# Performance work log

Hardware: AMD Instinct MI355X
Metric: run time of the kernel (lower is better)

Reference implementation:

```python
import jax, jax.numpy as jnp
import numpy as np

B, L, D_MODEL, D_FF, N_EXPERTS, TOP_K = 32, 256, 512, 2048, 8, 2
EPS = 1e-9


def setup_inputs() -> dict:
    key = jax.random.key(0)
    ks = jax.random.split(key, 7)
    scale1 = 1.0 / np.sqrt(D_MODEL)
    scale2 = 1.0 / np.sqrt(D_FF)
    return {
        "cycle_curve_data": jax.random.normal(ks[0], (B, L, D_MODEL), jnp.float32),
        "logits": jax.random.normal(ks[1], (B, N_EXPERTS), jnp.float32),
        "moe_masks": jax.random.randint(ks[2], (B, N_EXPERTS), 0, 2, jnp.int32),
        "W1": jax.random.normal(ks[3], (N_EXPERTS, D_MODEL, D_FF), jnp.float32) * scale1,
        "b1": jax.random.normal(ks[4], (N_EXPERTS, D_FF), jnp.float32) * scale1,
        "W2": jax.random.normal(ks[5], (N_EXPERTS, D_FF, D_MODEL), jnp.float32) * scale2,
        "b2": jax.random.normal(ks[6], (N_EXPERTS, D_MODEL), jnp.float32) * scale2,
    }


def _gates(logits, moe_masks):
    # softmax over experts, zero out unavailable experts, keep top-k, renormalize
    mask = (moe_masks == 1).astype(logits.dtype)               # [B, E]
    p = jax.nn.softmax(logits, axis=1) * mask                  # [B, E]
    _, idx = jax.lax.top_k(p, TOP_K)                           # [B, K]
    topk_mask = jnp.zeros_like(p).at[jnp.arange(p.shape[0])[:, None], idx].set(1.0)
    p = p * topk_mask
    return p / (jnp.sum(p, axis=1, keepdims=True) + EPS)       # [B, E]


def reference(cycle_curve_data, logits, moe_masks, W1, b1, W2, b2):
    gates = _gates(logits, moe_masks)                          # [B, E]
    x = cycle_curve_data                                       # [B, L, D]
    # dense equivalent of per-expert gather -> MLP -> gate-weighted scatter-combine
    h = jnp.einsum("bld,edf->eblf", x, W1) + b1[:, None, None, :]   # [E,B,L,F]
    h = jax.nn.gelu(h, approximate=False)
    out = jnp.einsum("be,eblf,efd->bld", gates, h, W2)
    out = out + jnp.einsum("be,ed->bd", gates, b2)[:, None, :]      # [B,L,D]
    return out
```

## Files before the change

### kernel.cpp

```cpp
#include <hip/hip_runtime.h>

#define B_SZ 32
#define L_SZ 256
#define D_SZ 512
#define F_SZ 2048
#define E_SZ 8
#define P_SZ 64
#define BK2  32

typedef __attribute__((ext_vector_type(8)))  short bf16x8;
typedef __attribute__((ext_vector_type(16))) float f32x16;

__device__ __forceinline__ unsigned short f2bf(float f) {
  unsigned int u = __builtin_bit_cast(unsigned int, f);
  u += 0x7fffu + ((u >> 16) & 1u);
  return (unsigned short)(u >> 16);
}

__device__ __forceinline__ void async16(const void* g, void* l) {
  __builtin_amdgcn_global_load_lds(
      (const __attribute__((address_space(1))) unsigned int*)g,
      (__attribute__((address_space(3))) unsigned int*)l, 16, 0, 0);
}

__device__ __forceinline__ float gelu_f(float x) {
  float a = fabsf(x) * 0.70710678118654752f;
  float t = __builtin_amdgcn_rcpf(1.0f + 0.3275911f * a);
  float y = t * (0.254829592f +
            t * (-0.284496736f +
            t * (1.421413741f +
            t * (-1.453152027f +
            t * 1.061405429f))));
  float e = __expf(-a * a);
  float erf_abs = 1.0f - y * e;
  float erf_v = (x < 0.f) ? -erf_abs : erf_abs;
  return 0.5f * x * (1.0f + erf_v);
}

#define PREP_CONV_BLKS 4096
#define PREP_TR_BLKS   2048
#define PREP_TOTAL     (1 + PREP_CONV_BLKS + 2 * PREP_TR_BLKS)

__global__ __launch_bounds__(256) void prep_kernel(
    const float* __restrict__ logits, const int* __restrict__ masks,
    const float* __restrict__ x,
    const float* __restrict__ W1, const float* __restrict__ W2,
    int* __restrict__ sel_e, float* __restrict__ sel_g,
    unsigned short* __restrict__ xb,
    unsigned short* __restrict__ w1t, unsigned short* __restrict__ w2t) {
  __shared__ float tile[64][65];
  int blk = blockIdx.x;
  int tid = threadIdx.x;

  if (blk == 0) {
    int b = tid;
    if (b >= B_SZ) return;
    float lg[E_SZ], p[E_SZ];
    float mx = -1e30f;
    for (int e = 0; e < E_SZ; ++e) { lg[e] = logits[b * E_SZ + e]; mx = fmaxf(mx, lg[e]); }
    float s = 0.f;
    for (int e = 0; e < E_SZ; ++e) { p[e] = expf(lg[e] - mx); s += p[e]; }
    for (int e = 0; e < E_SZ; ++e) p[e] = (masks[b * E_SZ + e] == 1) ? (p[e] / s) : 0.f;
    int i0 = 0, i1 = 1; float v0 = -1.f, v1 = -1.f;
    for (int e = 0; e < E_SZ; ++e) {
      float v = p[e];
      if (v > v0)      { v1 = v0; i1 = i0; v0 = v; i0 = e; }
      else if (v > v1) { v1 = v;  i1 = e; }
    }
    float den = v0 + v1 + 1e-9f;
    sel_e[2 * b] = i0;  sel_e[2 * b + 1] = i1;
    sel_g[2 * b] = v0 / den;
    sel_g[2 * b + 1] = v1 / den;
    return;
  }
  blk -= 1;

  if (blk < PREP_CONV_BLKS) {
    int i = blk * 256 + tid;
    float4 v = ((const float4*)x)[i];
    ushort4 o;
    o.x = f2bf(v.x); o.y = f2bf(v.y); o.z = f2bf(v.z); o.w = f2bf(v.w);
    ((ushort4*)xb)[i] = o;
    return;
  }
  blk -= PREP_CONV_BLKS;

  const float* in; unsigned short* out; int R, C, ls;
  if (blk < PREP_TR_BLKS) { in = W1; out = w1t; R = D_SZ; C = F_SZ; ls = 5; }
  else { blk -= PREP_TR_BLKS; in = W2; out = w2t; R = F_SZ; C = D_SZ; ls = 3; }
  int z = blk >> 8;
  int rem = blk & 255;
  int tr = rem >> ls, tc = rem & ((1 << ls) - 1);
  int r0 = tr * 64, c0 = tc * 64;
  const float* ip = in + (size_t)z * R * C;
  unsigned short* op = out + (size_t)z * C * R;
  int tx = tid & 63, ty = tid >> 6;
#pragma unroll
  for (int i = 0; i < 16; ++i) {
    int r = i * 4 + ty;
    tile[r][tx] = ip[(size_t)(r0 + r) * C + c0 + tx];
  }
  __syncthreads();
#pragma unroll
  for (int uu = 0; uu < 4; ++uu) {
    int u = uu * 256 + tid;
    int cc = u >> 4, q = u & 15;
    ushort4 o;
    o.x = f2bf(tile[q * 4 + 0][cc]);
    o.y = f2bf(tile[q * 4 + 1][cc]);
    o.z = f2bf(tile[q * 4 + 2][cc]);
    o.w = f2bf(tile[q * 4 + 3][cc]);
    *(ushort4*)(op + (size_t)(c0 + cc) * R + r0 + q * 4) = o;
  }
}

__global__ __launch_bounds__(256, 4) void moe_gemm1(
    const unsigned short* __restrict__ Xb,
    const unsigned short* __restrict__ W1t,
    const float* __restrict__ b1,
    const int* __restrict__ sel_e,
    unsigned short* __restrict__ H) {
  __shared__ __align__(16) unsigned short As[2][128 * BK2];
  __shared__ __align__(16) unsigned short Bs[2][128 * BK2];

  int lin = blockIdx.x;
  int xcd = lin & 7;
  int f   = (lin >> 3) & 15;
  int grp = lin >> 7;
  int pl  = grp * 8 + xcd;
  int p   = pl >> 1;
  int l0  = (pl & 1) * 128;
  int f0  = f * 128;
  int b   = p >> 1;
  int e   = sel_e[p];

  int tid = threadIdx.x;
  int lane = tid & 63;
  int w = tid >> 6, wm = w & 1, wn = w >> 1;
  int m32 = lane & 31, kh = lane >> 5;

  const unsigned short* Abase = Xb  + ((size_t)b * L_SZ + l0) * D_SZ;
  const unsigned short* Bbase = W1t + ((size_t)e * F_SZ + f0) * D_SZ;

  int seg0 = w * 128 + lane;
  int row0 = seg0 >> 2, ks0 = (seg0 & 3) * 8;
  int seg1 = seg0 + 64;
  int row1 = seg1 >> 2, ks1 = (seg1 & 3) * 8;

  f32x16 acc[2][2] = {};

  for (int k0 = 0; k0 < D_SZ; k0 += 2 * BK2) {
#pragma unroll
    for (int h = 0; h < 2; ++h) {
      int kk = k0 + h * BK2;
      async16(Abase + (size_t)row0 * D_SZ + kk + ks0, &As[h][seg0 * 8]);
      async16(Abase + (size_t)row1 * D_SZ + kk + ks1, &As[h][seg1 * 8]);
      async16(Bbase + (size_t)row0 * D_SZ + kk + ks0, &Bs[h][seg0 * 8]);
      async16(Bbase + (size_t)row1 * D_SZ + kk + ks1, &Bs[h][seg1 * 8]);
    }
    __syncthreads();
#pragma unroll
    for (int h = 0; h < 2; ++h)
#pragma unroll
      for (int s = 0; s < 2; ++s) {
        int ko = s * 16 + kh * 8;
        bf16x8 a0 = *(const bf16x8*)&As[h][(wm * 64 +      m32) * BK2 + ko];
        bf16x8 a1 = *(const bf16x8*)&As[h][(wm * 64 + 32 + m32) * BK2 + ko];
        bf16x8 b0 = *(const bf16x8*)&Bs[h][(wn * 64 +      m32) * BK2 + ko];
        bf16x8 b1f = *(const bf16x8*)&Bs[h][(wn * 64 + 32 + m32) * BK2 + ko];
        acc[0][0] = __builtin_amdgcn_mfma_f32_32x32x16_bf16(a0, b0,  acc[0][0], 0, 0, 0);
        acc[0][1] = __builtin_amdgcn_mfma_f32_32x32x16_bf16(a0, b1f, acc[0][1], 0, 0, 0);
        acc[1][0] = __builtin_amdgcn_mfma_f32_32x32x16_bf16(a1, b0,  acc[1][0], 0, 0, 0);
        acc[1][1] = __builtin_amdgcn_mfma_f32_32x32x16_bf16(a1, b1f, acc[1][1], 0, 0, 0);
      }
    __syncthreads();
  }

  float b1v[2];
#pragma unroll
  for (int tj = 0; tj < 2; ++tj)
    b1v[tj] = b1[e * F_SZ + f0 + wn * 64 + tj * 32 + m32];

  unsigned short* Hp = H + ((size_t)p * L_SZ + l0) * F_SZ + f0;
#pragma unroll
  for (int ti = 0; ti < 2; ++ti)
#pragma unroll
    for (int tj = 0; tj < 2; ++tj) {
      int col = wn * 64 + tj * 32 + m32;
#pragma unroll
      for (int r = 0; r < 16; ++r) {
        int row = wm * 64 + ti * 32 + (r & 3) + 8 * (r >> 2) + 4 * kh;
        Hp[(size_t)row * F_SZ + col] = f2bf(gelu_f(acc[ti][tj][r] + b1v[tj]));
      }
    }
}

__global__ __launch_bounds__(256, 4) void moe_gemm2(
    const unsigned short* __restrict__ H,
    const unsigned short* __restrict__ W2t,
    const float* __restrict__ b2,
    const int* __restrict__ sel_e,
    const float* __restrict__ sel_g,
    float* __restrict__ part,
    float* __restrict__ Out) {
  __shared__ __align__(16) unsigned short As[2][128 * BK2];
  __shared__ __align__(16) unsigned short Bs[2][128 * BK2];

  int lin = blockIdx.x;
  int q   = lin & 7;
  int d   = (lin >> 3) & 3;
  int g8  = lin >> 5;
  int gg  = g8 * 8 + q;
  int p   = gg >> 1;
  int l0  = (gg & 1) * 128;
  int d0  = d * 128;
  int b   = p >> 1;
  int e   = sel_e[p];
  float g = sel_g[p];

  int tid = threadIdx.x;
  int lane = tid & 63;
  int w = tid >> 6, wm = w & 1, wn = w >> 1;
  int m32 = lane & 31, kh = lane >> 5;

  const unsigned short* Abase = H   + ((size_t)p * L_SZ + l0) * F_SZ;
  const unsigned short* Bbase = W2t + ((size_t)e * D_SZ + d0) * F_SZ;

  int seg0 = w * 128 + lane;
  int row0 = seg0 >> 2, ks0 = (seg0 & 3) * 8;
  int seg1 = seg0 + 64;
  int row1 = seg1 >> 2, ks1 = (seg1 & 3) * 8;

  f32x16 acc[2][2] = {};

  for (int k0 = 0; k0 < F_SZ; k0 += 2 * BK2) {
#pragma unroll
    for (int h = 0; h < 2; ++h) {
      int kk = k0 + h * BK2;
      async16(Abase + (size_t)row0 * F_SZ + kk + ks0, &As[h][seg0 * 8]);
      async16(Abase + (size_t)row1 * F_SZ + kk + ks1, &As[h][seg1 * 8]);
      async16(Bbase + (size_t)row0 * F_SZ + kk + ks0, &Bs[h][seg0 * 8]);
      async16(Bbase + (size_t)row1 * F_SZ + kk + ks1, &Bs[h][seg1 * 8]);
    }
    __syncthreads();
#pragma unroll
    for (int h = 0; h < 2; ++h)
#pragma unroll
      for (int s = 0; s < 2; ++s) {
        int ko = s * 16 + kh * 8;
        bf16x8 a0 = *(const bf16x8*)&As[h][(wm * 64 +      m32) * BK2 + ko];
        bf16x8 a1 = *(const bf16x8*)&As[h][(wm * 64 + 32 + m32) * BK2 + ko];
        bf16x8 b0 = *(const bf16x8*)&Bs[h][(wn * 64 +      m32) * BK2 + ko];
        bf16x8 b1f = *(const bf16x8*)&Bs[h][(wn * 64 + 32 + m32) * BK2 + ko];
        acc[0][0] = __builtin_amdgcn_mfma_f32_32x32x16_bf16(a0, b0,  acc[0][0], 0, 0, 0);
        acc[0][1] = __builtin_amdgcn_mfma_f32_32x32x16_bf16(a0, b1f, acc[0][1], 0, 0, 0);
        acc[1][0] = __builtin_amdgcn_mfma_f32_32x32x16_bf16(a1, b0,  acc[1][0], 0, 0, 0);
        acc[1][1] = __builtin_amdgcn_mfma_f32_32x32x16_bf16(a1, b1f, acc[1][1], 0, 0, 0);
      }
    __syncthreads();
  }

  float bias[2] = {0.f, 0.f};
  if (p & 1) {
    int e0 = sel_e[2 * b], e1 = sel_e[2 * b + 1];
    float g0 = sel_g[2 * b], g1 = sel_g[2 * b + 1];
#pragma unroll
    for (int tj = 0; tj < 2; ++tj) {
      int dd = d0 + wn * 64 + tj * 32 + m32;
      bias[tj] = g0 * b2[e0 * D_SZ + dd] + g1 * b2[e1 * D_SZ + dd];
    }
  }
  float* dst = (p & 1) ? Out : part;
  float* Op = dst + ((size_t)b * L_SZ + l0) * D_SZ + d0;
#pragma unroll
  for (int ti = 0; ti < 2; ++ti)
#pragma unroll
    for (int tj = 0; tj < 2; ++tj) {
      int col = wn * 64 + tj * 32 + m32;
#pragma unroll
      for (int r = 0; r < 16; ++r) {
        int row = wm * 64 + ti * 32 + (r & 3) + 8 * (r >> 2) + 4 * kh;
        Op[(size_t)row * D_SZ + col] = g * acc[ti][tj][r] + bias[tj];
      }
    }
}

__global__ __launch_bounds__(256) void combine_kernel(
    const float* __restrict__ part, float* __restrict__ Out) {
  int i = blockIdx.x * 256 + threadIdx.x;
  float4 pv = ((const float4*)part)[i];
  float4 o  = ((float4*)Out)[i];
  o.x += pv.x; o.y += pv.y; o.z += pv.z; o.w += pv.w;
  ((float4*)Out)[i] = o;
}

extern "C" void kernel_launch(void* const* d_in, const int* in_sizes, int n_in,
                              void* d_out, int out_size, void* d_ws, size_t ws_size,
                              hipStream_t stream) {
  const float* x      = (const float*)d_in[0];
  const float* logits = (const float*)d_in[1];
  const int*   masks  = (const int*)d_in[2];
  const float* W1     = (const float*)d_in[3];
  const float* b1     = (const float*)d_in[4];
  const float* W2     = (const float*)d_in[5];
  const float* b2     = (const float*)d_in[6];
  float* out = (float*)d_out;

  char* ws = (char*)d_ws;
  int*   sel_e = (int*)ws;
  float* sel_g = (float*)(ws + 256);
  unsigned short* xb  = (unsigned short*)(ws + 1024);
  unsigned short* w1t = xb  + (size_t)B_SZ * L_SZ * D_SZ;
  unsigned short* w2t = w1t + (size_t)E_SZ * F_SZ * D_SZ;
  unsigned short* Hbuf = w2t + (size_t)E_SZ * D_SZ * F_SZ;
  float* part = (float*)(ws + 1024);

  prep_kernel<<<PREP_TOTAL, 256, 0, stream>>>(logits, masks, x, W1, W2,
                                              sel_e, sel_g, xb, w1t, w2t);
  moe_gemm1<<<2048, 256, 0, stream>>>(xb, w1t, b1, sel_e, Hbuf);
  moe_gemm2<<<512, 256, 0, stream>>>(Hbuf, w2t, b2, sel_e, sel_g, part, out);
  combine_kernel<<<(B_SZ * L_SZ * D_SZ / 4) / 256, 256, 0, stream>>>(part, out);
}
```

Baseline: 245.5 us.

## Overlap W2 transpose with GEMM1 and swizzle LDS tiles to avoid bank conflicts

Moves the W2 fp32-to-bf16 transpose out of the prep kernel and into extra blocks appended to the GEMM1 launch, so that work runs alongside GEMM1 instead of serially before it. Adds an XOR swizzle on the LDS k-chunk layout in both GEMMs to cut bank conflicts on the bf16x8 fragment reads. Also simplifies the GEMM1 block-to-tile mapping by dropping the XCD-aware remap. The tail transpose blocks use GEMM1's 32KB shared buffer and may compete with GEMM blocks for occupancy, and losing the XCD mapping may hurt L2 locality.

After: 226.1 us. 1.09x faster.

```diff
diff --git a/kernel.cpp b/kernel.cpp
--- a/kernel.cpp
+++ b/kernel.cpp
@@ -37,18 +37,41 @@
   return 0.5f * x * (1.0f + erf_v);
 }
 
+__device__ __forceinline__ void transpose_tile(
+    const float* __restrict__ ip, unsigned short* __restrict__ op,
+    int R, int C, int r0, int c0, float* tile, int tid) {
+  int tx = tid & 63, ty = tid >> 6;
+#pragma unroll
+  for (int i = 0; i < 16; ++i) {
+    int r = i * 4 + ty;
+    tile[r * 65 + tx] = ip[(size_t)(r0 + r) * C + c0 + tx];
+  }
+  __syncthreads();
+#pragma unroll
+  for (int uu = 0; uu < 4; ++uu) {
+    int u = uu * 256 + tid;
+    int cc = u >> 4, q = u & 15;
+    ushort4 o;
+    o.x = f2bf(tile[(q * 4 + 0) * 65 + cc]);
+    o.y = f2bf(tile[(q * 4 + 1) * 65 + cc]);
+    o.z = f2bf(tile[(q * 4 + 2) * 65 + cc]);
+    o.w = f2bf(tile[(q * 4 + 3) * 65 + cc]);
+    *(ushort4*)(op + (size_t)(c0 + cc) * R + r0 + q * 4) = o;
+  }
+}
+
 #define PREP_CONV_BLKS 4096
 #define PREP_TR_BLKS   2048
-#define PREP_TOTAL     (1 + PREP_CONV_BLKS + 2 * PREP_TR_BLKS)
+#define PREP_TOTAL     (1 + PREP_CONV_BLKS + PREP_TR_BLKS)
 
 __global__ __launch_bounds__(256) void prep_kernel(
     const float* __restrict__ logits, const int* __restrict__ masks,
     const float* __restrict__ x,
-    const float* __restrict__ W1, const float* __restrict__ W2,
+    const float* __restrict__ W1,
     int* __restrict__ sel_e, float* __restrict__ sel_g,
     unsigned short* __restrict__ xb,
-    unsigned short* __restrict__ w1t, unsigned short* __restrict__ w2t) {
-  __shared__ float tile[64][65];
+    unsigned short* __restrict__ w1t) {
+  __shared__ float tile[64 * 65];
   int blk = blockIdx.x;
   int tid = threadIdx.x;
 
@@ -85,33 +108,11 @@
   }
   blk -= PREP_CONV_BLKS;
 
-  const float* in; unsigned short* out; int R, C, ls;
-  if (blk < PREP_TR_BLKS) { in = W1; out = w1t; R = D_SZ; C = F_SZ; ls = 5; }
-  else { blk -= PREP_TR_BLKS; in = W2; out = w2t; R = F_SZ; C = D_SZ; ls = 3; }
   int z = blk >> 8;
   int rem = blk & 255;
-  int tr = rem >> ls, tc = rem & ((1 << ls) - 1);
-  int r0 = tr * 64, c0 = tc * 64;
-  const float* ip = in + (size_t)z * R * C;
-  unsigned short* op = out + (size_t)z * C * R;
-  int tx = tid & 63, ty = tid >> 6;
-#pragma unroll
-  for (int i = 0; i < 16; ++i) {
-    int r = i * 4 + ty;
-    tile[r][tx] = ip[(size_t)(r0 + r) * C + c0 + tx];
-  }
-  __syncthreads();
-#pragma unroll
-  for (int uu = 0; uu < 4; ++uu) {
-    int u = uu * 256 + tid;
-    int cc = u >> 4, q = u & 15;
-    ushort4 o;
-    o.x = f2bf(tile[q * 4 + 0][cc]);
-    o.y = f2bf(tile[q * 4 + 1][cc]);
-    o.z = f2bf(tile[q * 4 + 2][cc]);
-    o.w = f2bf(tile[q * 4 + 3][cc]);
-    *(ushort4*)(op + (size_t)(c0 + cc) * R + r0 + q * 4) = o;
-  }
+  int tr = rem >> 5, tc = rem & 31;
+  transpose_tile(W1 + (size_t)z * D_SZ * F_SZ, w1t + (size_t)z * D_SZ * F_SZ,
+                 D_SZ, F_SZ, tr * 64, tc * 64, tile, tid);
 }
 
 __global__ __launch_bounds__(256, 4) void moe_gemm1(
@@ -119,33 +120,45 @@
     const unsigned short* __restrict__ W1t,
     const float* __restrict__ b1,
     const int* __restrict__ sel_e,
-    unsigned short* __restrict__ H) {
-  __shared__ __align__(16) unsigned short As[2][128 * BK2];
-  __shared__ __align__(16) unsigned short Bs[2][128 * BK2];
-
+    unsigned short* __restrict__ H,
+    const float* __restrict__ W2,
+    unsigned short* __restrict__ w2t) {
+  __shared__ __align__(16) char smem[32768];
+  int tid = threadIdx.x;
   int lin = blockIdx.x;
-  int xcd = lin & 7;
-  int f   = (lin >> 3) & 15;
-  int grp = lin >> 7;
-  int pl  = grp * 8 + xcd;
-  int p   = pl >> 1;
-  int l0  = (pl & 1) * 128;
-  int f0  = f * 128;
-  int b   = p >> 1;
-  int e   = sel_e[p];
-
-  int tid = threadIdx.x;
+
+  if (lin >= 2048) {
+    int blk = lin - 2048;
+    int z = blk >> 8;
+    int rem = blk & 255;
+    int tr = rem >> 3, tc = rem & 7;
+    transpose_tile(W2 + (size_t)z * F_SZ * D_SZ, w2t + (size_t)z * F_SZ * D_SZ,
+                   F_SZ, D_SZ, tr * 64, tc * 64, (float*)smem, tid);
+    return;
+  }
+
+  unsigned short* As = (unsigned short*)smem;
+  unsigned short* Bs = (unsigned short*)(smem + 16384);
+
+  int f  = lin & 15;
+  int l0 = ((lin >> 4) & 1) * 128;
+  int p  = lin >> 5;
+  int f0 = f * 128;
+  int b  = p >> 1;
+  int e  = sel_e[p];
+
   int lane = tid & 63;
   int w = tid >> 6, wm = w & 1, wn = w >> 1;
   int m32 = lane & 31, kh = lane >> 5;
+  int sw = (m32 >> 1) & 3;
 
   const unsigned short* Abase = Xb  + ((size_t)b * L_SZ + l0) * D_SZ;
   const unsigned short* Bbase = W1t + ((size_t)e * F_SZ + f0) * D_SZ;
 
   int seg0 = w * 128 + lane;
-  int row0 = seg0 >> 2, ks0 = (seg0 & 3) * 8;
+  int row0 = seg0 >> 2, ks0 = ((seg0 & 3) ^ ((row0 >> 1) & 3)) * 8;
   int seg1 = seg0 + 64;
-  int row1 = seg1 >> 2, ks1 = (seg1 & 3) * 8;
+  int row1 = seg1 >> 2, ks1 = ((seg1 & 3) ^ ((row1 >> 1) & 3)) * 8;
 
   f32x16 acc[2][2] = {};
 
@@ -153,21 +166,21 @@
 #pragma unroll
     for (int h = 0; h < 2; ++h) {
       int kk = k0 + h * BK2;
-      async16(Abase + (size_t)row0 * D_SZ + kk + ks0, &As[h][seg0 * 8]);
-      async16(Abase + (size_t)row1 * D_SZ + kk + ks1, &As[h][seg1 * 8]);
-      async16(Bbase + (size_t)row0 * D_SZ + kk + ks0, &Bs[h][seg0 * 8]);
-      async16(Bbase + (size_t)row1 * D_SZ + kk + ks1, &Bs[h][seg1 * 8]);
+      async16(Abase + (size_t)row0 * D_SZ + kk + ks0, &As[(h * 512 + seg0) * 8]);
+      async16(Abase + (size_t)row1 * D_SZ + kk + ks1, &As[(h * 512 + seg1) * 8]);
+      async16(Bbase + (size_t)row0 * D_SZ + kk + ks0, &Bs[(h * 512 + seg0) * 8]);
+      async16(Bbase + (size_t)row1 * D_SZ + kk + ks1, &Bs[(h * 512 + seg1) * 8]);
     }
     __syncthreads();
 #pragma unroll
     for (int h = 0; h < 2; ++h)
 #pragma unroll
       for (int s = 0; s < 2; ++s) {
-        int ko = s * 16 + kh * 8;
-        bf16x8 a0 = *(const bf16x8*)&As[h][(wm * 64 +      m32) * BK2 + ko];
-        bf16x8 a1 = *(const bf16x8*)&As[h][(wm * 64 + 32 + m32) * BK2 + ko];
-        bf16x8 b0 = *(const bf16x8*)&Bs[h][(wn * 64 +      m32) * BK2 + ko];
-        bf16x8 b1f = *(const bf16x8*)&Bs[h][(wn * 64 + 32 + m32) * BK2 + ko];
+        int ko = ((((s << 1) | kh) ^ sw) << 3) + h * 4096;
+        bf16x8 a0  = *(const bf16x8*)&As[(wm * 64 +      m32) * BK2 + ko];
+        bf16x8 a1  = *(const bf16x8*)&As[(wm * 64 + 32 + m32) * BK2 + ko];
+        bf16x8 b0  = *(const bf16x8*)&Bs[(wn * 64 +      m32) * BK2 + ko];
+        bf16x8 b1f = *(const bf16x8*)&Bs[(wn * 64 + 32 + m32) * BK2 + ko];
         acc[0][0] = __builtin_amdgcn_mfma_f32_32x32x16_bf16(a0, b0,  acc[0][0], 0, 0, 0);
         acc[0][1] = __builtin_amdgcn_mfma_f32_32x32x16_bf16(a0, b1f, acc[0][1], 0, 0, 0);
         acc[1][0] = __builtin_amdgcn_mfma_f32_32x32x16_bf16(a1, b0,  acc[1][0], 0, 0, 0);
@@ -222,14 +235,15 @@
   int lane = tid & 63;
   int w = tid >> 6, wm = w & 1, wn = w >> 1;
   int m32 = lane & 31, kh = lane >> 5;
+  int sw = (m32 >> 1) & 3;
 
   const unsigned short* Abase = H   + ((size_t)p * L_SZ + l0) * F_SZ;
   const unsigned short* Bbase = W2t + ((size_t)e * D_SZ + d0) * F_SZ;
 
   int seg0 = w * 128 + lane;
-  int row0 = seg0 >> 2, ks0 = (seg0 & 3) * 8;
+  int row0 = seg0 >> 2, ks0 = ((seg0 & 3) ^ ((row0 >> 1) & 3)) * 8;
   int seg1 = seg0 + 64;
-  int row1 = seg1 >> 2, ks1 = (seg1 & 3) * 8;
+  int row1 = seg1 >> 2, ks1 = ((seg1 & 3) ^ ((row1 >> 1) & 3)) * 8;
 
   f32x16 acc[2][2] = {};
 
@@ -247,10 +261,10 @@
     for (int h = 0; h < 2; ++h)
 #pragma unroll
       for (int s = 0; s < 2; ++s) {
-        int ko = s * 16 + kh * 8;
-        bf16x8 a0 = *(const bf16x8*)&As[h][(wm * 64 +      m32) * BK2 + ko];
-        bf16x8 a1 = *(const bf16x8*)&As[h][(wm * 64 + 32 + m32) * BK2 + ko];
-        bf16x8 b0 = *(const bf16x8*)&Bs[h][(wn * 64 +      m32) * BK2 + ko];
+        int ko = (((s << 1) | kh) ^ sw) << 3;
+        bf16x8 a0  = *(const bf16x8*)&As[h][(wm * 64 +      m32) * BK2 + ko];
+        bf16x8 a1  = *(const bf16x8*)&As[h][(wm * 64 + 32 + m32) * BK2 + ko];
+        bf16x8 b0  = *(const bf16x8*)&Bs[h][(wn * 64 +      m32) * BK2 + ko];
         bf16x8 b1f = *(const bf16x8*)&Bs[h][(wn * 64 + 32 + m32) * BK2 + ko];
         acc[0][0] = __builtin_amdgcn_mfma_f32_32x32x16_bf16(a0, b0,  acc[0][0], 0, 0, 0);
         acc[0][1] = __builtin_amdgcn_mfma_f32_32x32x16_bf16(a0, b1f, acc[0][1], 0, 0, 0);
@@ -315,9 +329,9 @@
   unsigned short* Hbuf = w2t + (size_t)E_SZ * D_SZ * F_SZ;
   float* part = (float*)(ws + 1024);
 
-  prep_kernel<<<PREP_TOTAL, 256, 0, stream>>>(logits, masks, x, W1, W2,
-                                              sel_e, sel_g, xb, w1t, w2t);
-  moe_gemm1<<<2048, 256, 0, stream>>>(xb, w1t, b1, sel_e, Hbuf);
+  prep_kernel<<<PREP_TOTAL, 256, 0, stream>>>(logits, masks, x, W1,
+                                              sel_e, sel_g, xb, w1t);
+  moe_gemm1<<<4096, 256, 0, stream>>>(xb, w1t, b1, sel_e, Hbuf, W2, w2t);
   moe_gemm2<<<512, 256, 0, stream>>>(Hbuf, w2t, b2, sel_e, sel_g, part, out);
   combine_kernel<<<(B_SZ * L_SZ * D_SZ / 4) / 256, 256, 0, stream>>>(part, out);
 }
```
